# Performance work log

Measured on AMD Instinct MI355X. Metric: run time of the kernel, lower is better.

## Reference

```python
import jax, jax.numpy as jnp
import numpy as np

B, S, D, H, HD = 8, 1024, 1152, 16, 72
L, R = 32, 36  # get_decompose_dim(1152)
W_BITS, A_BITS = 4, 8


def _ste_round(x):
    return x + jax.lax.stop_gradient(jnp.round(x) - x)


def _fake_quant(x, bits):
    # symmetric fake quant, per last-dim group (per-token for acts, per-out-channel for weights)
    qmax = 2.0 ** (bits - 1) - 1.0
    scale = jnp.maximum(jnp.max(jnp.abs(x), axis=-1, keepdims=True) / qmax, 1e-8)
    return jnp.clip(_ste_round(x / scale), -qmax - 1.0, qmax) * scale


def _kron_apply(x, A, Bm):
    # DecomposeTransMatrix: x (..., L*R) -> reshape (L,R), Y = A^T X B (row-vector kron transform)
    sh = x.shape
    y = jnp.einsum('...lr,lp,rq->...pq', x.reshape(sh[:-1] + (L, R)), A, Bm)
    return y.reshape(sh)


def setup_inputs() -> dict:
    key = jax.random.key(0)
    ks = jax.random.split(key, 16)
    lin = lambda k, sh: jax.random.normal(k, sh, jnp.float32) * 0.02
    return {
        'hidden_states': jax.random.normal(ks[0], (B, S, D), jnp.float32),
        'Wq': lin(ks[1], (D, D)), 'bq': lin(ks[2], (D,)),
        'Wk': lin(ks[3], (D, D)), 'bk': lin(ks[4], (D,)),
        'Wv': lin(ks[5], (D, D)), 'bv': lin(ks[6], (D,)),
        'Wo': lin(ks[7], (D, D)), 'bo': lin(ks[8], (D,)),
        'ln_A': jnp.eye(L, dtype=jnp.float32) + 0.02 * jax.random.normal(ks[9], (L, L), jnp.float32),
        'ln_B': jnp.eye(R, dtype=jnp.float32) + 0.02 * jax.random.normal(ks[10], (R, R), jnp.float32),
        'ln_diag': 1.0 + 0.1 * jax.random.uniform(ks[11], (D,), jnp.float32),
        'vc': jnp.eye(HD, dtype=jnp.float32) + 0.02 * jax.random.normal(ks[12], (HD, HD), jnp.float32),
        'o_mat': jnp.eye(H, dtype=jnp.float32) + 0.02 * jax.random.normal(ks[13], (H, H), jnp.float32),
    }


def reference(hidden_states, Wq, bq, Wk, bk, Wv, bv, Wo, bo, ln_A, ln_B, ln_diag, vc, o_mat):
    invA_T = jnp.linalg.inv(ln_A).T
    invB_T = jnp.linalg.inv(ln_B).T
    # ln_trans applied to activations (diag scale + decomposed Kronecker rotation)
    x = _kron_apply(hidden_states * ln_diag, ln_A, ln_B)  # (B,S,D)

    def qlinear(xin, W, b, out_vc=None):
        # qa_trans inv_t folded into weight: W' = kron(W/diag, invA.T, invB.T) over input dim
        Wt = _kron_apply(W * (1.0 / ln_diag), invA_T, invB_T)
        bt = b
        if out_vc is not None:  # vc_trans folded into to_v output channels
            Wt = jnp.einsum('hdi,de->hei', Wt.reshape(H, HD, D), out_vc).reshape(D, D)
            bt = (b.reshape(H, HD) @ out_vc).reshape(-1)
        return _fake_quant(xin, A_BITS) @ _fake_quant(Wt, W_BITS).T + bt

    q = qlinear(x, Wq, bq).reshape(B, S, H, HD).transpose(0, 2, 1, 3)  # (B,H,S,HD)
    k = qlinear(x, Wk, bk).reshape(B, S, H, HD).transpose(0, 2, 1, 3)
    v = qlinear(x, Wv, bv, out_vc=vc).reshape(B, S, H, HD).transpose(0, 2, 1, 3)

    # baddbmm with beta=0, alpha=1: NO 1/sqrt(d) scaling (faithful to source)
    scores = jnp.einsum('bhqd,bhkd->bhqk', q, k)
    attn = jax.nn.softmax(scores.astype(jnp.float32), axis=-1).astype(q.dtype)
    ctx = jnp.einsum('bhqk,bhkd->bhqd', attn, v).transpose(0, 2, 1, 3)  # (B,S,H,HD)

    # o_trans: matmul(o_mat.T, Y) per token
    ctx = jnp.einsum('bsgd,gh->bshd', ctx, o_mat).reshape(B, S, D)

    # to_out with qa_trans=[inv(O).T, inv(V).T] folded into weight
    o_it = jnp.linalg.inv(o_mat).T
    v_it = jnp.linalg.inv(vc).T
    Wot = jnp.einsum('gh,ogd,de->ohe', o_it, Wo.reshape(D, H, HD), v_it).reshape(D, D)
    out = _fake_quant(ctx, A_BITS) @ _fake_quant(Wot, W_BITS).T + bo
    return out  # rescale_output_factor = 1.0
```

## Files before the change

kernel.cpp:

```cpp
#include <hip/hip_runtime.h>
#include <hip/hip_bf16.h>

#define BB 8
#define SS 1024
#define DD 1152
#define HH 16
#define HD 72
#define PD 96
#define LL 32
#define RR 36
#define NTOK (BB*SS)

typedef __attribute__((ext_vector_type(8)))  short short8;
typedef __attribute__((ext_vector_type(4)))  float f32x4;
typedef __attribute__((ext_vector_type(16))) float f32x16;
typedef __attribute__((ext_vector_type(4)))  unsigned short ushort4v;

#define F_IAT   0
#define F_IBT   1024
#define F_IO    2320
#define F_IV    2576
#define F_BVT   7760
#define F_SX    16384
#define F_SWQ   24576
#define F_SWK   25728
#define F_SWV   26880
#define F_SWO   28032
#define F_SCTX  32768
#define B_R1    1048576ULL
#define B_WB    (B_R1 + 37748736ULL)
#define B_XB    (B_WB + 4ULL*2654208ULL)
#define B_QB    (B_XB + 18874368ULL)
#define B_KB    (B_QB + 25165824ULL)
#define B_VB    (B_KB + 25165824ULL)
#define B_VT    (B_VB + 25165824ULL)
#define WSLOT   1327104ULL

__device__ __forceinline__ unsigned bf16rne(float f) {
    unsigned u = __builtin_bit_cast(unsigned, f);
    return (u + 0x7fffu + ((u >> 16) & 1u)) >> 16;
}
__device__ __forceinline__ unsigned cvtpk(float lo, float hi) {
    unsigned r;
    asm("v_cvt_pk_bf16_f32 %0, %1, %2" : "=v"(r) : "v"(lo), "v"(hi));
    return r;
}
__device__ __forceinline__ short8 mk8(unsigned a, unsigned b, unsigned c, unsigned d) {
    union { unsigned u[4]; short8 s; } t;
    t.u[0] = a; t.u[1] = b; t.u[2] = c; t.u[3] = d;
    return t.s;
}
__device__ __forceinline__ void async_ld16(void* lds, const void* g) {
    __builtin_amdgcn_global_load_lds((const __attribute__((address_space(1))) unsigned*)g,
                                     (__attribute__((address_space(3))) unsigned*)lds, 16, 0, 0);
}

__global__ void invert_kernel(const float* __restrict__ A32, const float* __restrict__ B36,
                              const float* __restrict__ O16, const float* __restrict__ V72,
                              float* __restrict__ ws)
{
    __shared__ float As[72][73], Xs[72][73], Ts[72][73], Us[72][73];
    int which = blockIdx.x;
    int n; const float* src;
    if (which == 0)      { n = 32; src = A32; }
    else if (which == 1) { n = 36; src = B36; }
    else if (which == 2) { n = 16; src = O16; }
    else                 { n = 72; src = V72; }
    int tid = threadIdx.x;
    for (int idx = tid; idx < n*n; idx += 256) {
        int i = idx / n, j = idx % n;
        float a = src[idx];
        As[i][j] = a;
        Xs[i][j] = (i == j ? 2.0f : 0.0f) - a;
    }
    __syncthreads();
    int ty = tid >> 5, tx = tid & 31;
    int j0 = tx, j1 = tx + 32, j2 = tx + 64;
    for (int step = 0; step < 4; ++step) {
        {
            float acc[9][3];
            #pragma unroll
            for (int a2 = 0; a2 < 9; ++a2) { acc[a2][0]=0.f; acc[a2][1]=0.f; acc[a2][2]=0.f; }
            for (int k = 0; k < n; ++k) {
                float b0 = (j0 < n) ? Xs[k][j0] : 0.f;
                float b1 = (j1 < n) ? Xs[k][j1] : 0.f;
                float b2 = (j2 < n) ? Xs[k][j2] : 0.f;
                #pragma unroll
                for (int a2 = 0; a2 < 9; ++a2) {
                    int i = ty + 8*a2;
                    float av = (i < n) ? As[i][k] : 0.f;
                    acc[a2][0] += av*b0; acc[a2][1] += av*b1; acc[a2][2] += av*b2;
                }
            }
            #pragma unroll
            for (int a2 = 0; a2 < 9; ++a2) {
                int i = ty + 8*a2;
                if (i < n) {
                    if (j0 < n) Ts[i][j0] = acc[a2][0];
                    if (j1 < n) Ts[i][j1] = acc[a2][1];
                    if (j2 < n) Ts[i][j2] = acc[a2][2];
                }
            }
        }
        __syncthreads();
        {
            float acc[9][3];
            #pragma unroll
            for (int a2 = 0; a2 < 9; ++a2) { acc[a2][0]=0.f; acc[a2][1]=0.f; acc[a2][2]=0.f; }
            for (int k = 0; k < n; ++k) {
                float b0 = (j0 < n) ? Ts[k][j0] : 0.f;
                float b1 = (j1 < n) ? Ts[k][j1] : 0.f;
                float b2 = (j2 < n) ? Ts[k][j2] : 0.f;
                #pragma unroll
                for (int a2 = 0; a2 < 9; ++a2) {
                    int i = ty + 8*a2;
                    float av = (i < n) ? Xs[i][k] : 0.f;
                    acc[a2][0] += av*b0; acc[a2][1] += av*b1; acc[a2][2] += av*b2;
                }
            }
            #pragma unroll
            for (int a2 = 0; a2 < 9; ++a2) {
                int i = ty + 8*a2;
                if (i < n) {
                    if (j0 < n) Us[i][j0] = acc[a2][0];
                    if (j1 < n) Us[i][j1] = acc[a2][1];
                    if (j2 < n) Us[i][j2] = acc[a2][2];
                }
            }
        }
        __syncthreads();
        for (int idx = tid; idx < n*n; idx += 256) {
            int i = idx / n, j = idx % n;
            Xs[i][j] = 2.0f*Xs[i][j] - Us[i][j];
        }
        __syncthreads();
    }
    if (which == 0) {
        for (int idx = tid; idx < 32*32; idx += 256) { int l = idx/32, pp = idx%32; ws[F_IAT + idx] = Xs[pp][l]; }
    } else if (which == 1) {
        for (int idx = tid; idx < 36*36; idx += 256) { int r = idx/36, qq = idx%36; ws[F_IBT + idx] = Xs[qq][r]; }
    } else if (which == 2) {
        for (int idx = tid; idx < 16*16; idx += 256) { int i = idx/16, j = idx%16; ws[F_IO + idx] = Xs[i][j]; }
    } else {
        for (int idx = tid; idx < 72*72; idx += 256) { int i = idx/72, j = idx%72; ws[F_IV + idx] = Xs[i][j]; }
    }
}

__global__ __launch_bounds__(256) void pad_zero(unsigned* __restrict__ qb, unsigned* __restrict__ kb)
{
    int idx = blockIdx.x*256 + threadIdx.x;
    int row = idx / 12, u = idx % 12;
    size_t off = (size_t)row*48 + 36 + u;
    qb[off] = 0u;
    kb[off] = 0u;
}

__global__ __launch_bounds__(256) void kron_act_q(const float* __restrict__ src, unsigned short* __restrict__ dst,
                                                  float* __restrict__ scl,
                                                  const float* __restrict__ P, const float* __restrict__ Q,
                                                  const float* __restrict__ diag)
{
    __shared__ float Xs[LL*RR], T1[LL*RR], Ps[LL*LL], Qs[RR*RR], Ys[LL*RR], red[256];
    int row = blockIdx.x;
    int tid = threadIdx.x;
    const float* sr = src + (size_t)row*DD;
    for (int i = tid; i < LL*LL; i += 256) Ps[i] = P[i];
    for (int i = tid; i < RR*RR; i += 256) Qs[i] = Q[i];
    for (int i = tid; i < DD; i += 256) Xs[i] = sr[i]*diag[i];
    __syncthreads();
    for (int s = tid; s < 288; s += 256) {
        int p = s / 9, r4 = (s % 9)*4;
        f32x4 acc = {0.f,0.f,0.f,0.f};
        #pragma unroll 8
        for (int l = 0; l < LL; ++l) {
            float a = Ps[l*LL + p];
            f32x4 x = *(const f32x4*)&Xs[l*RR + r4];
            acc += a*x;
        }
        *(f32x4*)&T1[p*RR + r4] = acc;
    }
    __syncthreads();
    float lmax = 0.f;
    for (int s = tid; s < 288; s += 256) {
        int p = s / 9, q4 = (s % 9)*4;
        f32x4 acc = {0.f,0.f,0.f,0.f};
        #pragma unroll 9
        for (int r = 0; r < RR; ++r) {
            float t = T1[p*RR + r];
            f32x4 qv = *(const f32x4*)&Qs[r*RR + q4];
            acc += t*qv;
        }
        *(f32x4*)&Ys[p*RR + q4] = acc;
        lmax = fmaxf(lmax, fmaxf(fmaxf(fabsf(acc[0]), fabsf(acc[1])), fmaxf(fabsf(acc[2]), fabsf(acc[3]))));
    }
    red[tid] = lmax; __syncthreads();
    for (int s = 128; s > 0; s >>= 1) { if (tid < s) red[tid] = fmaxf(red[tid], red[tid+s]); __syncthreads(); }
    float scale = fmaxf(red[0]/127.f, 1e-8f);
    float rs = 1.f/scale;
    if (tid == 0) scl[row] = scale;
    for (int s = tid; s < 288; s += 256) {
        int i4 = s*4;
        f32x4 y = *(const f32x4*)&Ys[i4];
        ushort4v o;
        #pragma unroll
        for (int c = 0; c < 4; ++c) {
            float v = rintf(y[c]*rs);
            v = fminf(fmaxf(v, -128.f), 127.f);
            o[c] = (unsigned short)bf16rne(v);
        }
        *(ushort4v*)&dst[(size_t)row*DD + i4] = o;
    }
}

__global__ __launch_bounds__(256) void kron_w_q(const float* __restrict__ src, unsigned short* __restrict__ dst,
                                                float* __restrict__ scl,
                                                const float* __restrict__ P, const float* __restrict__ Q,
                                                const float* __restrict__ diag)
{
    __shared__ float Xs[LL*RR], T1[LL*RR], Ps[LL*LL], Qs[RR*RR], Ys[LL*RR], red[256];
    int row = blockIdx.x;
    int tid = threadIdx.x;
    const float* sr = src + (size_t)row*DD;
    for (int i = tid; i < LL*LL; i += 256) Ps[i] = P[i];
    for (int i = tid; i < RR*RR; i += 256) Qs[i] = Q[i];
    for (int i = tid; i < DD; i += 256) Xs[i] = sr[i]*(1.0f/diag[i]);
    __syncthreads();
    for (int s = tid; s < 288; s += 256) {
        int p = s / 9, r4 = (s % 9)*4;
        f32x4 acc = {0.f,0.f,0.f,0.f};
        #pragma unroll 8
        for (int l = 0; l < LL; ++l) {
            float a = Ps[l*LL + p];
            f32x4 x = *(const f32x4*)&Xs[l*RR + r4];
            acc += a*x;
        }
        *(f32x4*)&T1[p*RR + r4] = acc;
    }
    __syncthreads();
    float lmax = 0.f;
    for (int s = tid; s < 288; s += 256) {
        int p = s / 9, q4 = (s % 9)*4;
        f32x4 acc = {0.f,0.f,0.f,0.f};
        #pragma unroll 9
        for (int r = 0; r < RR; ++r) {
            float t = T1[p*RR + r];
            f32x4 qv = *(const f32x4*)&Qs[r*RR + q4];
            acc += t*qv;
        }
        *(f32x4*)&Ys[p*RR + q4] = acc;
        lmax = fmaxf(lmax, fmaxf(fmaxf(fabsf(acc[0]), fabsf(acc[1])), fmaxf(fabsf(acc[2]), fabsf(acc[3]))));
    }
    red[tid] = lmax; __syncthreads();
    for (int s = 128; s > 0; s >>= 1) { if (tid < s) red[tid] = fmaxf(red[tid], red[tid+s]); __syncthreads(); }
    float scale = fmaxf(red[0]/7.f, 1e-8f);
    float rs = 1.f/scale;
    if (tid == 0) scl[row] = scale;
    for (int s = tid; s < 288; s += 256) {
        int i4 = s*4;
        f32x4 y = *(const f32x4*)&Ys[i4];
        ushort4v o;
        #pragma unroll
        for (int c = 0; c < 4; ++c) {
            float v = rintf(y[c]*rs);
            v = fminf(fmaxf(v, -8.f), 7.f);
            o[c] = (unsigned short)bf16rne(v);
        }
        *(ushort4v*)&dst[(size_t)row*DD + i4] = o;
    }
}

__global__ __launch_bounds__(256) void kron_rows(const float* __restrict__ src, float* __restrict__ dst,
                                                 const float* __restrict__ P, const float* __restrict__ Q,
                                                 const float* __restrict__ diag)
{
    __shared__ float Xs[LL*RR], T1[LL*RR], Ps[LL*LL], Qs[RR*RR];
    int row = blockIdx.x;
    int tid = threadIdx.x;
    const float* sr = src + (size_t)row*DD;
    for (int i = tid; i < LL*LL; i += 256) Ps[i] = P[i];
    for (int i = tid; i < RR*RR; i += 256) Qs[i] = Q[i];
    for (int i = tid; i < DD; i += 256) Xs[i] = sr[i]*(1.0f/diag[i]);
    __syncthreads();
    for (int s = tid; s < 288; s += 256) {
        int p = s / 9, r4 = (s % 9)*4;
        f32x4 acc = {0.f,0.f,0.f,0.f};
        #pragma unroll 8
        for (int l = 0; l < LL; ++l) {
            float a = Ps[l*LL + p];
            f32x4 x = *(const f32x4*)&Xs[l*RR + r4];
            acc += a*x;
        }
        *(f32x4*)&T1[p*RR + r4] = acc;
    }
    __syncthreads();
    for (int s = tid; s < 288; s += 256) {
        int p = s / 9, q4 = (s % 9)*4;
        f32x4 acc = {0.f,0.f,0.f,0.f};
        #pragma unroll 9
        for (int r = 0; r < RR; ++r) {
            float t = T1[p*RR + r];
            f32x4 qv = *(const f32x4*)&Qs[r*RR + q4];
            acc += t*qv;
        }
        *(f32x4*)&dst[(size_t)row*DD + p*RR + q4] = acc;
    }
}

__global__ __launch_bounds__(256) void wv_fold_q(const float* __restrict__ tmp, const float* __restrict__ vc,
                                                 const float* __restrict__ bv, unsigned short* __restrict__ dst,
                                                 float* __restrict__ scl, float* __restrict__ bvt)
{
    int he = blockIdx.x;
    int h = he / HD, e = he % HD;
    __shared__ float vcol[HD], Ys[DD], red[256];
    int tid = threadIdx.x;
    if (tid < HD) vcol[tid] = vc[tid*HD + e];
    __syncthreads();
    const float* base = tmp + (size_t)h*HD*DD;
    float lmax = 0.f;
    for (int i = tid; i < DD; i += 256) {
        float acc = 0.f;
        #pragma unroll 8
        for (int d = 0; d < HD; ++d) acc += base[(size_t)d*DD + i]*vcol[d];
        Ys[i] = acc;
        lmax = fmaxf(lmax, fabsf(acc));
    }
    red[tid] = lmax; __syncthreads();
    for (int s = 128; s > 0; s >>= 1) { if (tid < s) red[tid] = fmaxf(red[tid], red[tid+s]); __syncthreads(); }
    float scale = fmaxf(red[0]/7.f, 1e-8f);
    float rs = 1.f/scale;
    if (tid == 0) {
        scl[he] = scale;
        float acc = 0.f;
        for (int d = 0; d < HD; ++d) acc += bv[h*HD + d]*vcol[d];
        bvt[he] = acc;
    }
    for (int i = tid; i < DD; i += 256) {
        float v = rintf(Ys[i]*rs);
        v = fminf(fmaxf(v, -8.f), 7.f);
        dst[(size_t)he*DD + i] = (unsigned short)bf16rne(v);
    }
}

__global__ __launch_bounds__(256) void wo_trans_q(const float* __restrict__ Wo, const float* __restrict__ iO,
                                                  const float* __restrict__ iV, unsigned short* __restrict__ dst,
                                                  float* __restrict__ scl)
{
    __shared__ float M[HH*HD], T1[HH*HD], iOs[HH*HH], iVs[HD*HD], Ys[DD], red[256];
    int row = blockIdx.x, tid = threadIdx.x;
    for (int i = tid; i < DD; i += 256) M[i] = Wo[(size_t)row*DD + i];
    for (int i = tid; i < HH*HH; i += 256) iOs[i] = iO[i];
    for (int i = tid; i < HD*HD; i += 256) iVs[i] = iV[i];
    __syncthreads();
    for (int i = tid; i < DD; i += 256) {
        int h = i / HD, d = i % HD;
        float a = 0.f;
        #pragma unroll
        for (int g = 0; g < HH; ++g) a += iOs[h*HH + g]*M[g*HD + d];
        T1[i] = a;
    }
    __syncthreads();
    float lmax = 0.f;
    for (int i = tid; i < DD; i += 256) {
        int h = i / HD, e = i % HD;
        float a = 0.f;
        #pragma unroll 8
        for (int d = 0; d < HD; ++d) a += T1[h*HD + d]*iVs[e*HD + d];
        Ys[i] = a;
        lmax = fmaxf(lmax, fabsf(a));
    }
    red[tid] = lmax; __syncthreads();
    for (int s = 128; s > 0; s >>= 1) { if (tid < s) red[tid] = fmaxf(red[tid], red[tid+s]); __syncthreads(); }
    float scale = fmaxf(red[0]/7.f, 1e-8f);
    float rs = 1.f/scale;
    if (tid == 0) scl[row] = scale;
    for (int i = tid; i < DD; i += 256) {
        float v = rintf(Ys[i]*rs);
        v = fminf(fmaxf(v, -8.f), 7.f);
        dst[(size_t)row*DD + i] = (unsigned short)bf16rne(v);
    }
}

__device__ __forceinline__ void gemm_body(const unsigned short* __restrict__ Xb, const unsigned short* __restrict__ Wb,
                                          unsigned short* As, unsigned short* Bs, f32x4 (&acc)[4][4],
                                          int wr, int wc, int lr, int lg)
{
    for (int k0 = 0; k0 < DD; k0 += 32) {
        int tid = threadIdx.x;
        #pragma unroll
        for (int j = 0; j < 2; ++j) {
            int idx = tid + j*256;
            int row = idx >> 2, pp = idx & 3;
            int s = pp ^ ((row >> 1) & 3);
            async_ld16(&As[idx*8], Xb + (size_t)row*DD + k0 + s*8);
            async_ld16(&Bs[idx*8], Wb + (size_t)row*DD + k0 + s*8);
        }
        __syncthreads();
        short8 a[4], bfr[4];
        #pragma unroll
        for (int fr = 0; fr < 4; ++fr) {
            int row = wr*64 + fr*16 + lr;
            a[fr] = *(const short8*)(&As[row*32 + (lg ^ ((row>>1)&3))*8]);
        }
        #pragma unroll
        for (int fc = 0; fc < 4; ++fc) {
            int row = wc*64 + fc*16 + lr;
            bfr[fc] = *(const short8*)(&Bs[row*32 + (lg ^ ((row>>1)&3))*8]);
        }
        #pragma unroll
        for (int fr = 0; fr < 4; ++fr)
            #pragma unroll
            for (int fc = 0; fc < 4; ++fc)
                acc[fr][fc] = __builtin_amdgcn_mfma_f32_16x16x32_bf16(a[fr], bfr[fc], acc[fr][fc], 0, 0, 0);
        __syncthreads();
    }
}

__global__ __launch_bounds__(256) void gemm_qkv(const unsigned short* __restrict__ X,
                                                const unsigned short* __restrict__ Wq_b,
                                                const unsigned short* __restrict__ Wk_b,
                                                const unsigned short* __restrict__ Wv_b,
                                                const float* __restrict__ sx, const float* __restrict__ ws_all,
                                                const float* __restrict__ bq, const float* __restrict__ bk,
                                                const float* __restrict__ bvt,
                                                unsigned short* __restrict__ qb, unsigned short* __restrict__ kb,
                                                unsigned short* __restrict__ vb)
{
    __shared__ unsigned short As[128*32];
    __shared__ unsigned short Bs[128*32];
    int bn = blockIdx.x, bm = blockIdx.y, z = blockIdx.z;
    const unsigned short* W = (z == 0) ? Wq_b : (z == 1) ? Wk_b : Wv_b;
    const float* sw_ = ws_all + (size_t)z*1152;
    const float* bias = (z == 0) ? bq : (z == 1) ? bk : bvt;
    unsigned short* outQ = (z == 0) ? qb : (z == 1) ? kb : vb;
    int tid = threadIdx.x;
    int wave = tid >> 6, lane = tid & 63;
    int wr = wave >> 1, wc = wave & 1;
    int lr = lane & 15, lg = lane >> 4;
    f32x4 acc[4][4];
    #pragma unroll
    for (int i = 0; i < 4; ++i)
        #pragma unroll
        for (int j = 0; j < 4; ++j)
            #pragma unroll
            for (int e = 0; e < 4; ++e) acc[i][j][e] = 0.f;
    gemm_body(X + (size_t)bm*128*DD, W + (size_t)bn*128*DD, As, Bs, acc, wr, wc, lr, lg);
    #pragma unroll
    for (int fc = 0; fc < 4; ++fc) {
        int n = bn*128 + wc*64 + fc*16 + lr;
        float swn = sw_[n], bnv = bias[n];
        int h = n/72, hd = n - (n/72)*72;
        #pragma unroll
        for (int fr = 0; fr < 4; ++fr) {
            #pragma unroll
            for (int j = 0; j < 4; ++j) {
                int mrow = bm*128 + wr*64 + fr*16 + lg*4 + j;
                float v = acc[fr][fc][j]*sx[mrow]*swn + bnv;
                int b = mrow >> 10, s = mrow & 1023;
                outQ[(((size_t)b*HH + h)*SS + s)*PD + hd] = (unsigned short)bf16rne(v);
            }
        }
    }
}

__global__ __launch_bounds__(256) void gemm_out(const unsigned short* __restrict__ X, const unsigned short* __restrict__ W,
                                                const float* __restrict__ sx, const float* __restrict__ sw_,
                                                const float* __restrict__ bias, float* __restrict__ outF)
{
    __shared__ unsigned short As[128*32];
    __shared__ unsigned short Bs[128*32];
    int bn = blockIdx.x, bm = blockIdx.y;
    int tid = threadIdx.x;
    int wave = tid >> 6, lane = tid & 63;
    int wr = wave >> 1, wc = wave & 1;
    int lr = lane & 15, lg = lane >> 4;
    f32x4 acc[4][4];
    #pragma unroll
    for (int i = 0; i < 4; ++i)
        #pragma unroll
        for (int j = 0; j < 4; ++j)
            #pragma unroll
            for (int e = 0; e < 4; ++e) acc[i][j][e] = 0.f;
    gemm_body(X + (size_t)bm*128*DD, W + (size_t)bn*128*DD, As, Bs, acc, wr, wc, lr, lg);
    #pragma unroll
    for (int fc = 0; fc < 4; ++fc) {
        int n = bn*128 + wc*64 + fc*16 + lr;
        float swn = sw_[n], bnv = bias[n];
        #pragma unroll
        for (int fr = 0; fr < 4; ++fr) {
            #pragma unroll
            for (int j = 0; j < 4; ++j) {
                int mrow = bm*128 + wr*64 + fr*16 + lg*4 + j;
                outF[(size_t)mrow*DD + n] = acc[fr][fc][j]*sx[mrow]*swn + bnv;
            }
        }
    }
}

__global__ __launch_bounds__(256) void transpose_v(const unsigned short* __restrict__ v, unsigned short* __restrict__ vT)
{
    __shared__ unsigned short t[64][100];
    int head = blockIdx.x >> 4, st = blockIdx.x & 15;
    int tid = threadIdx.x;
    const unsigned short* src = v + ((size_t)head*SS + st*64)*PD;
    for (int idx = tid; idx < 64*PD; idx += 256) {
        int i = idx / PD, d = idx % PD;
        t[i][d] = src[idx];
    }
    __syncthreads();
    unsigned short* dst = vT + (size_t)head*PD*SS + st*64;
    for (int idx = tid; idx < PD*64; idx += 256) {
        int d = idx >> 6, i = idx & 63;
        dst[(size_t)d*SS + i] = t[i][d];
    }
}

__global__ __launch_bounds__(256) void attn_mfma(const unsigned short* __restrict__ q, const unsigned short* __restrict__ k,
                                                 const unsigned short* __restrict__ vT, float* __restrict__ ctx)
{
    __shared__ unsigned short Kl[64*128];
    __shared__ unsigned short Vl[96*64];
    int blk = blockIdx.x;
    int bh = blk >> 3;
    int qblk = blk & 7;
    int tid = threadIdx.x;
    int wave = tid >> 6, lane = tid & 63;
    int lq = lane & 31, half = lane >> 5;
    int b = bh >> 4, h = bh & 15;
    const unsigned short* qbase = q + ((size_t)bh*SS + qblk*128 + wave*32)*PD;
    const unsigned short* kbase = k + (size_t)bh*SS*PD;
    const unsigned short* vtb   = vT + (size_t)bh*PD*SS;
    short8 qf[6];
    #pragma unroll
    for (int ks = 0; ks < 6; ++ks)
        qf[ks] = *(const short8*)(qbase + (size_t)lq*PD + ks*16 + half*8);
    f32x16 O0, O1, O2;
    #pragma unroll
    for (int r = 0; r < 16; ++r) { O0[r] = 0.f; O1[r] = 0.f; O2[r] = 0.f; }
    float m = -1e30f, l = 0.f;
    for (int t0 = 0; t0 < SS; t0 += 64) {
        __syncthreads();
        #pragma unroll
        for (int j = 0; j < 3; ++j) {
            int idx = tid + j*256;
            int row = idx / 12, s = idx % 12;
            int phys = s ^ (row & 7);
            short8 val = *(const short8*)(kbase + (size_t)(t0 + row)*PD + s*8);
            *(short8*)(&Kl[row*128 + phys*8]) = val;
        }
        #pragma unroll
        for (int j = 0; j < 3; ++j) {
            int idx = tid + j*256;
            int d = idx >> 3, p = idx & 7;
            int s = p ^ (d & 7);
            short8 val = *(const short8*)(vtb + (size_t)d*SS + t0 + s*8);
            *(short8*)(&Vl[d*64 + p*8]) = val;
        }
        __syncthreads();
        #pragma unroll
        for (int sub = 0; sub < 2; ++sub) {
            f32x16 sacc;
            #pragma unroll
            for (int r = 0; r < 16; ++r) sacc[r] = 0.f;
            #pragma unroll
            for (int ks = 0; ks < 6; ++ks) {
                int key = sub*32 + lq;
                short8 kf = *(const short8*)(&Kl[key*128 + (((ks*2 + half) ^ (lq & 7)))*8]);
                sacc = __builtin_amdgcn_mfma_f32_32x32x16_bf16(kf, qf[ks], sacc, 0, 0, 0);
            }
            float pa = fmaxf(fmaxf(sacc[0], sacc[1]), fmaxf(sacc[2], sacc[3]));
            float pb = fmaxf(fmaxf(sacc[4], sacc[5]), fmaxf(sacc[6], sacc[7]));
            float pc = fmaxf(fmaxf(sacc[8], sacc[9]), fmaxf(sacc[10], sacc[11]));
            float pd = fmaxf(fmaxf(sacc[12], sacc[13]), fmaxf(sacc[14], sacc[15]));
            float pmax = fmaxf(fmaxf(pa, pb), fmaxf(pc, pd));
            pmax = fmaxf(pmax, __shfl_xor(pmax, 32));
            if (!__all(pmax - m <= 8.0f)) {
                float mn = fmaxf(m, pmax);
                float corr = __expf(m - mn);
                m = mn;
                l *= corr;
                #pragma unroll
                for (int r = 0; r < 16; ++r) {
                    int rowq = (r&3) + 8*(r>>2) + 4*half;
                    float cr = __shfl(corr, rowq);
                    O0[r] *= cr; O1[r] *= cr; O2[r] *= cr;
                }
            }
            float p[16]; float ls = 0.f;
            #pragma unroll
            for (int r = 0; r < 16; ++r) { p[r] = __expf(sacc[r] - m); ls += p[r]; }
            ls += __shfl_xor(ls, 32);
            l += ls;
            unsigned pk[8], sw[8];
            #pragma unroll
            for (int j2 = 0; j2 < 8; ++j2) pk[j2] = cvtpk(p[2*j2], p[2*j2+1]);
            #pragma unroll
            for (int j2 = 0; j2 < 8; ++j2) sw[j2] = __shfl_xor(pk[j2], 32);
            short8 A0 = half ? mk8(sw[2], sw[3], pk[2], pk[3]) : mk8(pk[0], pk[1], sw[0], sw[1]);
            short8 A1 = half ? mk8(sw[6], sw[7], pk[6], pk[7]) : mk8(pk[4], pk[5], sw[4], sw[5]);
            #pragma unroll
            for (int dt = 0; dt < 3; ++dt) {
                int d = dt*32 + lq;
                short8 vf0 = *(const short8*)(&Vl[d*64 + (((sub*4 + half) ^ (d & 7)))*8]);
                short8 vf1 = *(const short8*)(&Vl[d*64 + (((sub*4 + 2 + half) ^ (d & 7)))*8]);
                if (dt == 0) { O0 = __builtin_amdgcn_mfma_f32_32x32x16_bf16(A0, vf0, O0, 0,0,0);
                               O0 = __builtin_amdgcn_mfma_f32_32x32x16_bf16(A1, vf1, O0, 0,0,0); }
                if (dt == 1) { O1 = __builtin_amdgcn_mfma_f32_32x32x16_bf16(A0, vf0, O1, 0,0,0);
                               O1 = __builtin_amdgcn_mfma_f32_32x32x16_bf16(A1, vf1, O1, 0,0,0); }
                if (dt == 2) { O2 = __builtin_amdgcn_mfma_f32_32x32x16_bf16(A0, vf0, O2, 0,0,0);
                               O2 = __builtin_amdgcn_mfma_f32_32x32x16_bf16(A1, vf1, O2, 0,0,0); }
            }
        }
    }
    float linv = 1.f / l;
    #pragma unroll
    for (int r = 0; r < 16; ++r) {
        int rowq = (r&3) + 8*(r>>2) + 4*half;
        float lr = __shfl(linv, rowq);
        int s = qblk*128 + wave*32 + rowq;
        size_t base = ((size_t)(b*SS + s))*DD + h*HD;
        ctx[base + lq]      = O0[r]*lr;
        ctx[base + 32 + lq] = O1[r]*lr;
        if (lq < 8) ctx[base + 64 + lq] = O2[r]*lr;
    }
}

__global__ __launch_bounds__(256) void octx_fq_q(const float* __restrict__ ctx, const float* __restrict__ o_mat,
                                                 unsigned short* __restrict__ out, float* __restrict__ scl)
{
    __shared__ float ct[DD], Ys[DD], om[HH*HH], red[256];
    int t = blockIdx.x, tid = threadIdx.x;
    for (int i = tid; i < DD; i += 256) ct[i] = ctx[(size_t)t*DD + i];
    for (int i = tid; i < HH*HH; i += 256) om[i] = o_mat[i];
    __syncthreads();
    float lmax = 0.f;
    for (int s = tid; s < 288; s += 256) {
        int h = s / 18, d4 = (s % 18)*4;
        f32x4 acc = {0.f,0.f,0.f,0.f};
        #pragma unroll
        for (int g = 0; g < HH; ++g) {
            float o = om[g*HH + h];
            f32x4 c = *(const f32x4*)&ct[g*HD + d4];
            acc += o*c;
        }
        *(f32x4*)&Ys[h*HD + d4] = acc;
        lmax = fmaxf(lmax, fmaxf(fmaxf(fabsf(acc[0]), fabsf(acc[1])), fmaxf(fabsf(acc[2]), fabsf(acc[3]))));
    }
    red[tid] = lmax; __syncthreads();
    for (int s = 128; s > 0; s >>= 1) { if (tid < s) red[tid] = fmaxf(red[tid], red[tid+s]); __syncthreads(); }
    float scale = fmaxf(red[0]/127.f, 1e-8f);
    float rs = 1.f/scale;
    if (tid == 0) scl[t] = scale;
    for (int s = tid; s < 288; s += 256) {
        int i4 = s*4;
        f32x4 y = *(const f32x4*)&Ys[i4];
        ushort4v o;
        #pragma unroll
        for (int c = 0; c < 4; ++c) {
            float v = rintf(y[c]*rs);
            v = fminf(fmaxf(v, -128.f), 127.f);
            o[c] = (unsigned short)bf16rne(v);
        }
        *(ushort4v*)&out[(size_t)t*DD + i4] = o;
    }
}

extern "C" void kernel_launch(void* const* d_in, const int* in_sizes, int n_in,
                              void* d_out, int out_size, void* d_ws, size_t ws_size,
                              hipStream_t stream)
{
    const float* hidden = (const float*)d_in[0];
    const float* Wq = (const float*)d_in[1];  const float* bq = (const float*)d_in[2];
    const float* Wk = (const float*)d_in[3];  const float* bk = (const float*)d_in[4];
    const float* Wv = (const float*)d_in[5];  const float* bv = (const float*)d_in[6];
    const float* Wo = (const float*)d_in[7];  const float* bo = (const float*)d_in[8];
    const float* lnA = (const float*)d_in[9];
    const float* lnB = (const float*)d_in[10];
    const float* ln_diag = (const float*)d_in[11];
    const float* vc = (const float*)d_in[12];
    const float* o_mat = (const float*)d_in[13];
    float* ws = (float*)d_ws;
    float* out = (float*)d_out;
    char* wsb = (char*)d_ws;

    float* iAT  = ws + F_IAT;
    float* iBT  = ws + F_IBT;
    float* iO   = ws + F_IO;
    float* iV   = ws + F_IV;
    float* bvt  = ws + F_BVT;
    float* s_x  = ws + F_SX;
    float* s_wq = ws + F_SWQ;
    float* s_wk = ws + F_SWK;
    float* s_wv = ws + F_SWV;
    float* s_wo = ws + F_SWO;
    float* s_ct = ws + F_SCTX;

    float* slot = (float*)(wsb + B_R1);
    float* Wvm  = slot + 2*WSLOT;
    float* ctxf = slot;

    unsigned short* Wq_b = (unsigned short*)(wsb + B_WB);
    unsigned short* Wk_b = Wq_b + WSLOT;
    unsigned short* Wv_b = Wq_b + 2*WSLOT;
    unsigned short* Wo_b = Wq_b + 3*WSLOT;
    unsigned short* x_b  = (unsigned short*)(wsb + B_XB);
    unsigned short* ctx_b = x_b;
    unsigned short* qb = (unsigned short*)(wsb + B_QB);
    unsigned short* kb = (unsigned short*)(wsb + B_KB);
    unsigned short* vb = (unsigned short*)(wsb + B_VB);
    unsigned short* vT = (unsigned short*)(wsb + B_VT);

    invert_kernel<<<4, 256, 0, stream>>>(lnA, lnB, o_mat, vc, ws);
    kron_act_q<<<NTOK, 256, 0, stream>>>(hidden, x_b, s_x, lnA, lnB, ln_diag);
    kron_w_q<<<DD, 256, 0, stream>>>(Wq, Wq_b, s_wq, iAT, iBT, ln_diag);
    kron_w_q<<<DD, 256, 0, stream>>>(Wk, Wk_b, s_wk, iAT, iBT, ln_diag);
    kron_rows<<<DD, 256, 0, stream>>>(Wv, Wvm, iAT, iBT, ln_diag);
    wv_fold_q<<<DD, 256, 0, stream>>>(Wvm, vc, bv, Wv_b, s_wv, bvt);
    wo_trans_q<<<DD, 256, 0, stream>>>(Wo, iO, iV, Wo_b, s_wo);
    pad_zero<<<(131072*12)/256, 256, 0, stream>>>((unsigned*)qb, (unsigned*)kb);
    dim3 ggrid(DD/128, NTOK/128, 3);
    gemm_qkv<<<ggrid, 256, 0, stream>>>(x_b, Wq_b, Wk_b, Wv_b, s_x, s_wq, bq, bk, bvt, qb, kb, vb);
    transpose_v<<<BB*HH*16, 256, 0, stream>>>(vb, vT);
    attn_mfma<<<BB*HH*8, 256, 0, stream>>>(qb, kb, vT, ctxf);
    octx_fq_q<<<NTOK, 256, 0, stream>>>(ctxf, o_mat, ctx_b, s_ct);
    dim3 ogrid(DD/128, NTOK/128);
    gemm_out<<<ogrid, 256, 0, stream>>>(ctx_b, Wo_b, s_ct, s_wo, bo, out);
}
```

Measured before the change: 686.9 us.

## Use higher-order Newton-Schulz inversion and fuse Q/K pad zeroing into QKV GEMM

The matrix-inverse kernel moves from four second-order Newton-Schulz steps to two third-order steps. It uses vectorized float4 register tiling with 128 threads, which cuts the number of serial small GEMMs and barriers in a single-block kernel sitting on the critical path. The separate pad_zero launch is removed, and the bn==0 QKV GEMM blocks now zero the padding columns of q/k. That saves a kernel launch and a pass over memory, but it changes convergence behaviour and adds a small amount of work to some GEMM blocks.

```diff
diff --git a/kernel.cpp b/kernel.cpp
--- a/kernel.cpp
+++ b/kernel.cpp
@@ -55,11 +55,11 @@
                                      (__attribute__((address_space(3))) unsigned*)lds, 16, 0, 0);
 }
 
-__global__ void invert_kernel(const float* __restrict__ A32, const float* __restrict__ B36,
-                              const float* __restrict__ O16, const float* __restrict__ V72,
-                              float* __restrict__ ws)
-{
-    __shared__ float As[72][73], Xs[72][73], Ts[72][73], Us[72][73];
+__global__ __launch_bounds__(128) void invert_kernel(const float* __restrict__ A32, const float* __restrict__ B36,
+                                                     const float* __restrict__ O16, const float* __restrict__ V72,
+                                                     float* __restrict__ ws)
+{
+    __shared__ float As[80*76], Xs[80*76], Ys[80*76], Ps[80*76], Wt[80*76];
     int which = blockIdx.x;
     int n; const float* src;
     if (which == 0)      { n = 32; src = A32; }
@@ -67,92 +67,81 @@
     else if (which == 2) { n = 16; src = O16; }
     else                 { n = 72; src = V72; }
     int tid = threadIdx.x;
-    for (int idx = tid; idx < n*n; idx += 256) {
+    int nq = n >> 2;
+    for (int idx = tid; idx < n*n; idx += 128) {
         int i = idx / n, j = idx % n;
         float a = src[idx];
-        As[i][j] = a;
-        Xs[i][j] = (i == j ? 2.0f : 0.0f) - a;
-    }
-    __syncthreads();
-    int ty = tid >> 5, tx = tid & 31;
-    int j0 = tx, j1 = tx + 32, j2 = tx + 64;
-    for (int step = 0; step < 4; ++step) {
-        {
-            float acc[9][3];
-            #pragma unroll
-            for (int a2 = 0; a2 < 9; ++a2) { acc[a2][0]=0.f; acc[a2][1]=0.f; acc[a2][2]=0.f; }
-            for (int k = 0; k < n; ++k) {
-                float b0 = (j0 < n) ? Xs[k][j0] : 0.f;
-                float b1 = (j1 < n) ? Xs[k][j1] : 0.f;
-                float b2 = (j2 < n) ? Xs[k][j2] : 0.f;
-                #pragma unroll
-                for (int a2 = 0; a2 < 9; ++a2) {
-                    int i = ty + 8*a2;
-                    float av = (i < n) ? As[i][k] : 0.f;
-                    acc[a2][0] += av*b0; acc[a2][1] += av*b1; acc[a2][2] += av*b2;
-                }
-            }
-            #pragma unroll
-            for (int a2 = 0; a2 < 9; ++a2) {
-                int i = ty + 8*a2;
-                if (i < n) {
-                    if (j0 < n) Ts[i][j0] = acc[a2][0];
-                    if (j1 < n) Ts[i][j1] = acc[a2][1];
-                    if (j2 < n) Ts[i][j2] = acc[a2][2];
-                }
-            }
-        }
-        __syncthreads();
-        {
-            float acc[9][3];
-            #pragma unroll
-            for (int a2 = 0; a2 < 9; ++a2) { acc[a2][0]=0.f; acc[a2][1]=0.f; acc[a2][2]=0.f; }
-            for (int k = 0; k < n; ++k) {
-                float b0 = (j0 < n) ? Ts[k][j0] : 0.f;
-                float b1 = (j1 < n) ? Ts[k][j1] : 0.f;
-                float b2 = (j2 < n) ? Ts[k][j2] : 0.f;
-                #pragma unroll
-                for (int a2 = 0; a2 < 9; ++a2) {
-                    int i = ty + 8*a2;
-                    float av = (i < n) ? Xs[i][k] : 0.f;
-                    acc[a2][0] += av*b0; acc[a2][1] += av*b1; acc[a2][2] += av*b2;
-                }
-            }
-            #pragma unroll
-            for (int a2 = 0; a2 < 9; ++a2) {
-                int i = ty + 8*a2;
-                if (i < n) {
-                    if (j0 < n) Us[i][j0] = acc[a2][0];
-                    if (j1 < n) Us[i][j1] = acc[a2][1];
-                    if (j2 < n) Us[i][j2] = acc[a2][2];
-                }
-            }
-        }
-        __syncthreads();
-        for (int idx = tid; idx < n*n; idx += 256) {
-            int i = idx / n, j = idx % n;
-            Xs[i][j] = 2.0f*Xs[i][j] - Us[i][j];
-        }
-        __syncthreads();
-    }
+        As[i*76 + j] = a;
+        Xs[i*76 + j] = (i == j ? 2.0f : 0.0f) - a;
+    }
+    __syncthreads();
+    int ty = tid >> 3, qq = tid & 7;
+
+#define NSGEMM(DST, SA, SB) { \
+    f32x4 c00={0,0,0,0},c01={0,0,0,0},c02={0,0,0,0}, \
+          c10={0,0,0,0},c11={0,0,0,0},c12={0,0,0,0}, \
+          c20={0,0,0,0},c21={0,0,0,0},c22={0,0,0,0}, \
+          c30={0,0,0,0},c31={0,0,0,0},c32={0,0,0,0}, \
+          c40={0,0,0,0},c41={0,0,0,0},c42={0,0,0,0}; \
+    _Pragma("unroll 2") \
+    for (int k = 0; k < n; ++k) { \
+        const float* sb = &SB[k*76]; \
+        f32x4 b0 = *(const f32x4*)(sb + 4*qq); \
+        f32x4 b1 = *(const f32x4*)(sb + 4*qq + 32); \
+        f32x4 b2 = *(const f32x4*)(sb + 4*qq + 64); \
+        float a0 = SA[ty*76 + k]; \
+        float a1 = SA[(ty+16)*76 + k]; \
+        float a2 = SA[(ty+32)*76 + k]; \
+        float a3 = SA[(ty+48)*76 + k]; \
+        float a4 = SA[(ty+64)*76 + k]; \
+        c00 += a0*b0; c01 += a0*b1; c02 += a0*b2; \
+        c10 += a1*b0; c11 += a1*b1; c12 += a1*b2; \
+        c20 += a2*b0; c21 += a2*b1; c22 += a2*b2; \
+        c30 += a3*b0; c31 += a3*b1; c32 += a3*b2; \
+        c40 += a4*b0; c41 += a4*b1; c42 += a4*b2; \
+    } \
+    { \
+        f32x4 cc[5][3] = {{c00,c01,c02},{c10,c11,c12},{c20,c21,c22},{c30,c31,c32},{c40,c41,c42}}; \
+        _Pragma("unroll") \
+        for (int m = 0; m < 5; ++m) { \
+            int i = ty + 16*m; \
+            if (i < n) { \
+                _Pragma("unroll") \
+                for (int c = 0; c < 3; ++c) { \
+                    int q = qq + 8*c; \
+                    if (q < nq) *(f32x4*)&DST[i*76 + 4*q] = cc[m][c]; \
+                } \
+            } \
+        } \
+    } \
+}
+
+#define NSELEM(PD_, YD_) { \
+    for (int idx = tid; idx < n*n; idx += 128) { \
+        int i = idx / n, j = idx % n; \
+        PD_[i*76 + j] = PD_[i*76 + j] - 3.0f*YD_[i*76 + j] + (i == j ? 3.0f : 0.0f); \
+    } \
+}
+    NSGEMM(Ys, As, Xs); __syncthreads();
+    NSGEMM(Ps, Ys, Ys); __syncthreads();
+    NSELEM(Ps, Ys);     __syncthreads();
+    NSGEMM(Wt, Xs, Ps); __syncthreads();
+    NSGEMM(Ys, As, Wt); __syncthreads();
+    NSGEMM(Ps, Ys, Ys); __syncthreads();
+    NSELEM(Ps, Ys);     __syncthreads();
+    NSGEMM(Xs, Wt, Ps); __syncthreads();
+#undef NSGEMM
+#undef NSELEM
+
     if (which == 0) {
-        for (int idx = tid; idx < 32*32; idx += 256) { int l = idx/32, pp = idx%32; ws[F_IAT + idx] = Xs[pp][l]; }
+        for (int idx = tid; idx < 32*32; idx += 128) { int l = idx/32, pp = idx%32; ws[F_IAT + idx] = Xs[pp*76 + l]; }
     } else if (which == 1) {
-        for (int idx = tid; idx < 36*36; idx += 256) { int r = idx/36, qq = idx%36; ws[F_IBT + idx] = Xs[qq][r]; }
+        for (int idx = tid; idx < 36*36; idx += 128) { int r = idx/36, qx = idx%36; ws[F_IBT + idx] = Xs[qx*76 + r]; }
     } else if (which == 2) {
-        for (int idx = tid; idx < 16*16; idx += 256) { int i = idx/16, j = idx%16; ws[F_IO + idx] = Xs[i][j]; }
+        for (int idx = tid; idx < 16*16; idx += 128) { int i = idx/16, j = idx%16; ws[F_IO + idx] = Xs[i*76 + j]; }
     } else {
-        for (int idx = tid; idx < 72*72; idx += 256) { int i = idx/72, j = idx%72; ws[F_IV + idx] = Xs[i][j]; }
-    }
-}
-
-__global__ __launch_bounds__(256) void pad_zero(unsigned* __restrict__ qb, unsigned* __restrict__ kb)
-{
-    int idx = blockIdx.x*256 + threadIdx.x;
-    int row = idx / 12, u = idx % 12;
-    size_t off = (size_t)row*48 + 36 + u;
-    qb[off] = 0u;
-    kb[off] = 0u;
+        for (int idx = tid; idx < 72*72; idx += 128) { int i = idx/72, j = idx%72; ws[F_IV + idx] = Xs[i*76 + j]; }
+    }
 }
 
 __global__ __launch_bounds__(256) void kron_act_q(const float* __restrict__ src, unsigned short* __restrict__ dst,
@@ -434,6 +423,16 @@
     const float* bias = (z == 0) ? bq : (z == 1) ? bk : bvt;
     unsigned short* outQ = (z == 0) ? qb : (z == 1) ? kb : vb;
     int tid = threadIdx.x;
+    if (bn == 0 && z <= 1) {
+        short8 zero = {0,0,0,0,0,0,0,0};
+        for (int t = tid; t < 6144; t += 256) {
+            int tok = t / 48, rem = t % 48;
+            int h = rem / 3, c = rem % 3;
+            int mrow = bm*128 + tok;
+            int b = mrow >> 10, s = mrow & 1023;
+            *(short8*)(&outQ[(((size_t)b*HH + h)*SS + s)*PD + 72 + c*8]) = zero;
+        }
+    }
     int wave = tid >> 6, lane = tid & 63;
     int wr = wave >> 1, wc = wave & 1;
     int lr = lane & 15, lg = lane >> 4;
@@ -710,14 +709,13 @@
     unsigned short* vb = (unsigned short*)(wsb + B_VB);
     unsigned short* vT = (unsigned short*)(wsb + B_VT);
 
-    invert_kernel<<<4, 256, 0, stream>>>(lnA, lnB, o_mat, vc, ws);
+    invert_kernel<<<4, 128, 0, stream>>>(lnA, lnB, o_mat, vc, ws);
     kron_act_q<<<NTOK, 256, 0, stream>>>(hidden, x_b, s_x, lnA, lnB, ln_diag);
     kron_w_q<<<DD, 256, 0, stream>>>(Wq, Wq_b, s_wq, iAT, iBT, ln_diag);
     kron_w_q<<<DD, 256, 0, stream>>>(Wk, Wk_b, s_wk, iAT, iBT, ln_diag);
     kron_rows<<<DD, 256, 0, stream>>>(Wv, Wvm, iAT, iBT, ln_diag);
     wv_fold_q<<<DD, 256, 0, stream>>>(Wvm, vc, bv, Wv_b, s_wv, bvt);
     wo_trans_q<<<DD, 256, 0, stream>>>(Wo, iO, iV, Wo_b, s_wo);
-    pad_zero<<<(131072*12)/256, 256, 0, stream>>>((unsigned*)qb, (unsigned*)kb);
     dim3 ggrid(DD/128, NTOK/128, 3);
     gemm_qkv<<<ggrid, 256, 0, stream>>>(x_b, Wq_b, Wk_b, Wv_b, s_x, s_wq, bq, bk, bvt, qb, kb, vb);
     transpose_v<<<BB*HH*16, 256, 0, stream>>>(vb, vT);
```

Measured after the change: 612.2 us. 1.12x faster.
